# Kernel optimization log

Measured on AMD Instinct MI355X. Metric: run time of the kernel, lower is better.

## Reference

```python
import jax, jax.numpy as jnp
import numpy as np


def setup_inputs() -> dict:
    key = jax.random.key(0)
    k1, k2, k3, k4 = jax.random.split(key, 4)
    B, S, D = 16, 1024, 300      # batch, set_size, word_vector_dim
    K = 64                        # hidden_set_size == compressed_dim (element_dim)
    O = 256                       # set_representation_dim (output_dim)
    Xs = jax.random.normal(k1, (B, S, D), dtype=jnp.float32)
    # Linear(word_vector_dim -> hidden_set_size)
    W = jax.random.normal(k2, (K, D), dtype=jnp.float32) * (1.0 / np.sqrt(D))
    b = jax.random.normal(k3, (K,), dtype=jnp.float32) * 0.01
    # hidden_sets: (output_dim, hidden_set_size, element_dim) with xavier-normal scale
    xav = np.sqrt(2.0 / (K + K))
    hidden_sets = jax.random.normal(k4, (O, K, K), dtype=jnp.float32) * xav
    return {"Xs": Xs, "W": W, "b": b, "hidden_sets": hidden_sets}


def reference(Xs, W, b, hidden_sets):
    # compress: [B,S,D] @ [D,K] + b -> [B,S,K]
    Xc = jnp.einsum('bsd,kd->bsk', Xs, W) + b
    # bipartite_match: tensordot over element_dim -> [B,S,O,N] (N = hidden_set_size)
    G = jax.nn.relu(jnp.einsum('bsk,onk->bson', Xc, hidden_sets))
    # set_size (1024) > hidden_set_size (64): max over hidden-set axis, sum over set axis
    value = jnp.sum(jnp.max(G, axis=-1), axis=1)  # [B,O]
    return value
```

## Files before the change

### kernel.cpp

```cpp
#include <hip/hip_runtime.h>
#include <hip/hip_bf16.h>

#define B_  16
#define S_  1024
#define D_  300
#define DP  320
#define K_  64
#define O_  256
#define M_  (B_*S_)

typedef __attribute__((ext_vector_type(8)))  short s8b;
typedef __attribute__((ext_vector_type(4)))  float f32x4;
typedef __attribute__((ext_vector_type(16))) float f32x16;

#define MFMA16(a,b,c) __builtin_amdgcn_mfma_f32_16x16x32_bf16((a),(b),(c),0,0,0)
#define MFMA32(a,b,c) __builtin_amdgcn_mfma_f32_32x32x16_bf16((a),(b),(c),0,0,0)

__device__ __forceinline__ unsigned short bf16_bits(float f) {
    return __builtin_bit_cast(unsigned short, __float2bfloat16(f));
}

#define XS_BLK 2560
#define H_BLK  512
#define W_BLK  10
__global__ __launch_bounds__(256) void k_convert(
        const float* __restrict__ Xs, const float* __restrict__ W,
        const float* __restrict__ H,
        __hip_bfloat16* __restrict__ Xsb, __hip_bfloat16* __restrict__ Wb,
        __hip_bfloat16* __restrict__ Hb) {
    int bx = blockIdx.x, t = threadIdx.x;
    const float* src; __hip_bfloat16* dst; int r, c;
    if (bx < XS_BLK) {
        int g = bx * 256 + t;
        r = g / 40; c = (g - r * 40) * 8;
        src = Xs + (size_t)r * D_; dst = Xsb + (size_t)r * DP + c;
    } else if (bx < XS_BLK + H_BLK) {
        int g = ((bx - XS_BLK) * 256 + t) * 8;
        float4 f0 = *(const float4*)(H + g);
        float4 f1 = *(const float4*)(H + g + 4);
        union { unsigned short us[8]; uint4 q; } pk;
        pk.us[0]=bf16_bits(f0.x); pk.us[1]=bf16_bits(f0.y);
        pk.us[2]=bf16_bits(f0.z); pk.us[3]=bf16_bits(f0.w);
        pk.us[4]=bf16_bits(f1.x); pk.us[5]=bf16_bits(f1.y);
        pk.us[6]=bf16_bits(f1.z); pk.us[7]=bf16_bits(f1.w);
        *(uint4*)(Hb + g) = pk.q;
        return;
    } else {
        int g = (bx - XS_BLK - H_BLK) * 256 + t;
        r = g / 40; c = (g - r * 40) * 8;
        src = W + (size_t)r * D_; dst = Wb + (size_t)r * DP + c;
    }
    float v[8];
    if (c + 8 <= D_) {
        float4 f0 = *(const float4*)(src + c);
        float4 f1 = *(const float4*)(src + c + 4);
        v[0]=f0.x; v[1]=f0.y; v[2]=f0.z; v[3]=f0.w;
        v[4]=f1.x; v[5]=f1.y; v[6]=f1.z; v[7]=f1.w;
    } else {
#pragma unroll
        for (int j = 0; j < 8; ++j) v[j] = (c + j < D_) ? src[c + j] : 0.0f;
    }
    union { unsigned short us[8]; uint4 q; } pk;
#pragma unroll
    for (int j = 0; j < 8; ++j) pk.us[j] = bf16_bits(v[j]);
    *(uint4*)dst = pk.q;
}

__global__ __launch_bounds__(256) void k_compress(
        const __hip_bfloat16* __restrict__ Xsb,
        const __hip_bfloat16* __restrict__ Wb,
        const float* __restrict__ bias,
        __hip_bfloat16* __restrict__ Xc) {
    int tid  = threadIdx.x;
    int w    = tid >> 6, lane = tid & 63;
    int q    = lane >> 4, r = lane & 15;
    int row0 = blockIdx.x * 16;
    int col0 = w * 16;

    f32x4 acc0 = {0.f,0.f,0.f,0.f}, acc1 = {0.f,0.f,0.f,0.f};
    const __hip_bfloat16* arow = Xsb + (size_t)(row0 + r) * DP;
    const __hip_bfloat16* brow = Wb  + (size_t)(col0 + r) * DP;

#pragma unroll
    for (int ks = 0; ks < 5; ++ks) {
        int k0 = (2 * ks) * 32 + q * 8;
        int k1 = (2 * ks + 1) * 32 + q * 8;
        s8b a0 = __builtin_bit_cast(s8b, *(const uint4*)(arow + k0));
        s8b b0 = __builtin_bit_cast(s8b, *(const uint4*)(brow + k0));
        acc0 = MFMA16(a0, b0, acc0);
        s8b a1 = __builtin_bit_cast(s8b, *(const uint4*)(arow + k1));
        s8b b1 = __builtin_bit_cast(s8b, *(const uint4*)(brow + k1));
        acc1 = MFMA16(a1, b1, acc1);
    }
#pragma unroll
    for (int i = 0; i < 4; ++i) {
        int orow = row0 + q * 4 + i;
        int c    = col0 + r;
        Xc[(size_t)orow * K_ + c] =
            __float2bfloat16(acc0[i] + acc1[i] + bias[c]);
    }
}

__global__ __launch_bounds__(256, 4) void k_fused(
        const __hip_bfloat16* __restrict__ Xc,
        const __hip_bfloat16* __restrict__ Hb,
        float* __restrict__ out) {
    __shared__ __hip_bfloat16 lx[256 * 64];
    int tid   = threadIdx.x;
    int w     = tid >> 6, lane = tid & 63;
    int half  = lane >> 5, l31 = lane & 31;
    int bx    = blockIdx.x;
    int rb    = bx >> 6;
    int oq    = bx & 63;
    int o     = oq * 4 + w;
    int row0  = rb * 256;
    int batch = rb >> 2;

    {
        int r0 = tid >> 3, c = tid & 7;
#pragma unroll
        for (int i = 0; i < 8; ++i) {
            int r = r0 + i * 32;
            uint4 v = *(const uint4*)(Xc + (size_t)(row0 + r) * 64 + c * 8);
            *(uint4*)(&lx[r * 64 + (c ^ (r & 7)) * 8]) = v;
        }
    }

    s8b af[2][4];
#pragma unroll
    for (int nt = 0; nt < 2; ++nt) {
        const __hip_bfloat16* hrow =
            Hb + (size_t)(o * 64 + nt * 32 + l31) * 64 + half * 8;
#pragma unroll
        for (int ks = 0; ks < 4; ++ks)
            af[nt][ks] = __builtin_bit_cast(s8b, *(const uint4*)(hrow + ks * 16));
    }
    __syncthreads();

    float total = 0.0f;
#pragma unroll
    for (int t = 0; t < 8; ++t) {
        int rr = t * 32 + l31;
        int sw = rr & 7;
        s8b bf[4];
#pragma unroll
        for (int ks = 0; ks < 4; ++ks)
            bf[ks] = __builtin_bit_cast(s8b,
                *(const uint4*)(&lx[rr * 64 + ((2 * ks + half) ^ sw) * 8]));

        f32x16 a0 = {0.f,0.f,0.f,0.f,0.f,0.f,0.f,0.f,
                     0.f,0.f,0.f,0.f,0.f,0.f,0.f,0.f};
        f32x16 a1 = a0;
#pragma unroll
        for (int ks = 0; ks < 4; ++ks) {
            a0 = MFMA32(af[0][ks], bf[ks], a0);
            a1 = MFMA32(af[1][ks], bf[ks], a1);
        }
        float m0 = fmaxf(fmaxf(a0[0], a0[1]),  fmaxf(a0[2], a0[3]));
        float m1 = fmaxf(fmaxf(a0[4], a0[5]),  fmaxf(a0[6], a0[7]));
        float m2 = fmaxf(fmaxf(a0[8], a0[9]),  fmaxf(a0[10], a0[11]));
        float m3 = fmaxf(fmaxf(a0[12], a0[13]),fmaxf(a0[14], a0[15]));
        float n0 = fmaxf(fmaxf(a1[0], a1[1]),  fmaxf(a1[2], a1[3]));
        float n1 = fmaxf(fmaxf(a1[4], a1[5]),  fmaxf(a1[6], a1[7]));
        float n2 = fmaxf(fmaxf(a1[8], a1[9]),  fmaxf(a1[10], a1[11]));
        float n3 = fmaxf(fmaxf(a1[12], a1[13]),fmaxf(a1[14], a1[15]));
        float v  = fmaxf(fmaxf(fmaxf(m0, m1), fmaxf(m2, m3)),
                         fmaxf(fmaxf(n0, n1), fmaxf(n2, n3)));
        v = fmaxf(v, __shfl_xor(v, 32));
        v = fmaxf(v, 0.0f);
        total += v;
    }
    total += __shfl_xor(total, 1);
    total += __shfl_xor(total, 2);
    total += __shfl_xor(total, 4);
    total += __shfl_xor(total, 8);
    total += __shfl_xor(total, 16);
    if (lane == 0) atomicAdd(out + batch * O_ + o, total);
}

extern "C" void kernel_launch(void* const* d_in, const int* in_sizes, int n_in,
                              void* d_out, int out_size, void* d_ws, size_t ws_size,
                              hipStream_t stream) {
    const float* Xs   = (const float*)d_in[0];
    const float* W    = (const float*)d_in[1];
    const float* bias = (const float*)d_in[2];
    const float* H    = (const float*)d_in[3];
    float* out = (float*)d_out;

    char* ws = (char*)d_ws;
    __hip_bfloat16* Xsb = (__hip_bfloat16*)(ws);
    __hip_bfloat16* Wb  = (__hip_bfloat16*)(ws + 10485760);
    __hip_bfloat16* Hb  = (__hip_bfloat16*)(ws + 10526720);
    __hip_bfloat16* Xc  = (__hip_bfloat16*)(ws + 12623872);

    hipMemsetAsync(d_out, 0, (size_t)out_size * sizeof(float), stream);
    k_convert <<<XS_BLK + H_BLK + W_BLK, 256, 0, stream>>>(Xs, W, H, Xsb, Wb, Hb);
    k_compress<<<M_ / 16, 256, 0, stream>>>(Xsb, Wb, bias, Xc);
    k_fused   <<<64 * 64, 256, 0, stream>>>(Xc, Hb, out);
}
```

Before: 125.5 us.

## Fuse Xs bf16 conversion into compress and loop fused kernel over whole batch

```diff
diff --git a/kernel.cpp b/kernel.cpp
--- a/kernel.cpp
+++ b/kernel.cpp
@@ -20,22 +20,14 @@
     return __builtin_bit_cast(unsigned short, __float2bfloat16(f));
 }
 
-#define XS_BLK 2560
 #define H_BLK  512
 #define W_BLK  10
 __global__ __launch_bounds__(256) void k_convert(
-        const float* __restrict__ Xs, const float* __restrict__ W,
-        const float* __restrict__ H,
-        __hip_bfloat16* __restrict__ Xsb, __hip_bfloat16* __restrict__ Wb,
-        __hip_bfloat16* __restrict__ Hb) {
+        const float* __restrict__ W, const float* __restrict__ H,
+        __hip_bfloat16* __restrict__ Wb, __hip_bfloat16* __restrict__ Hb) {
     int bx = blockIdx.x, t = threadIdx.x;
-    const float* src; __hip_bfloat16* dst; int r, c;
-    if (bx < XS_BLK) {
-        int g = bx * 256 + t;
-        r = g / 40; c = (g - r * 40) * 8;
-        src = Xs + (size_t)r * D_; dst = Xsb + (size_t)r * DP + c;
-    } else if (bx < XS_BLK + H_BLK) {
-        int g = ((bx - XS_BLK) * 256 + t) * 8;
+    if (bx < H_BLK) {
+        int g = (bx * 256 + t) * 8;
         float4 f0 = *(const float4*)(H + g);
         float4 f1 = *(const float4*)(H + g + 4);
         union { unsigned short us[8]; uint4 q; } pk;
@@ -45,11 +37,10 @@
         pk.us[6]=bf16_bits(f1.z); pk.us[7]=bf16_bits(f1.w);
         *(uint4*)(Hb + g) = pk.q;
         return;
-    } else {
-        int g = (bx - XS_BLK - H_BLK) * 256 + t;
-        r = g / 40; c = (g - r * 40) * 8;
-        src = W + (size_t)r * D_; dst = Wb + (size_t)r * DP + c;
-    }
+    }
+    int g = (bx - H_BLK) * 256 + t;
+    int r = g / 40, c = (g - r * 40) * 8;
+    const float* src = W + (size_t)r * D_;
     float v[8];
     if (c + 8 <= D_) {
         float4 f0 = *(const float4*)(src + c);
@@ -63,11 +54,11 @@
     union { unsigned short us[8]; uint4 q; } pk;
 #pragma unroll
     for (int j = 0; j < 8; ++j) pk.us[j] = bf16_bits(v[j]);
-    *(uint4*)dst = pk.q;
+    *(uint4*)(Wb + (size_t)r * DP + c) = pk.q;
 }
 
 __global__ __launch_bounds__(256) void k_compress(
-        const __hip_bfloat16* __restrict__ Xsb,
+        const float* __restrict__ Xs,
         const __hip_bfloat16* __restrict__ Wb,
         const float* __restrict__ bias,
         __hip_bfloat16* __restrict__ Xc) {
@@ -78,19 +69,23 @@
     int col0 = w * 16;
 
     f32x4 acc0 = {0.f,0.f,0.f,0.f}, acc1 = {0.f,0.f,0.f,0.f};
-    const __hip_bfloat16* arow = Xsb + (size_t)(row0 + r) * DP;
-    const __hip_bfloat16* brow = Wb  + (size_t)(col0 + r) * DP;
-
-#pragma unroll
-    for (int ks = 0; ks < 5; ++ks) {
-        int k0 = (2 * ks) * 32 + q * 8;
-        int k1 = (2 * ks + 1) * 32 + q * 8;
-        s8b a0 = __builtin_bit_cast(s8b, *(const uint4*)(arow + k0));
-        s8b b0 = __builtin_bit_cast(s8b, *(const uint4*)(brow + k0));
-        acc0 = MFMA16(a0, b0, acc0);
-        s8b a1 = __builtin_bit_cast(s8b, *(const uint4*)(arow + k1));
-        s8b b1 = __builtin_bit_cast(s8b, *(const uint4*)(brow + k1));
-        acc1 = MFMA16(a1, b1, acc1);
+    const float*          arow = Xs + (size_t)(row0 + r) * D_;
+    const __hip_bfloat16* brow = Wb + (size_t)(col0 + r) * DP;
+    const float4 z4 = {0.f,0.f,0.f,0.f};
+
+#pragma unroll
+    for (int ks = 0; ks < 10; ++ks) {
+        int k0 = ks * 32 + q * 8;
+        float4 f0 = (k0     < D_) ? *(const float4*)(arow + k0)     : z4;
+        float4 f1 = (k0 + 4 < D_) ? *(const float4*)(arow + k0 + 4) : z4;
+        union { unsigned short us[8]; s8b v; } pk;
+        pk.us[0]=bf16_bits(f0.x); pk.us[1]=bf16_bits(f0.y);
+        pk.us[2]=bf16_bits(f0.z); pk.us[3]=bf16_bits(f0.w);
+        pk.us[4]=bf16_bits(f1.x); pk.us[5]=bf16_bits(f1.y);
+        pk.us[6]=bf16_bits(f1.z); pk.us[7]=bf16_bits(f1.w);
+        s8b b = __builtin_bit_cast(s8b, *(const uint4*)(brow + k0));
+        if (ks & 1) acc1 = MFMA16(pk.v, b, acc1);
+        else        acc0 = MFMA16(pk.v, b, acc0);
     }
 #pragma unroll
     for (int i = 0; i < 4; ++i) {
@@ -105,26 +100,14 @@
         const __hip_bfloat16* __restrict__ Xc,
         const __hip_bfloat16* __restrict__ Hb,
         float* __restrict__ out) {
-    __shared__ __hip_bfloat16 lx[256 * 64];
+    __shared__ __hip_bfloat16 lx[128 * 64];
     int tid   = threadIdx.x;
     int w     = tid >> 6, lane = tid & 63;
     int half  = lane >> 5, l31 = lane & 31;
     int bx    = blockIdx.x;
-    int rb    = bx >> 6;
+    int batch = bx >> 6;
     int oq    = bx & 63;
     int o     = oq * 4 + w;
-    int row0  = rb * 256;
-    int batch = rb >> 2;
-
-    {
-        int r0 = tid >> 3, c = tid & 7;
-#pragma unroll
-        for (int i = 0; i < 8; ++i) {
-            int r = r0 + i * 32;
-            uint4 v = *(const uint4*)(Xc + (size_t)(row0 + r) * 64 + c * 8);
-            *(uint4*)(&lx[r * 64 + (c ^ (r & 7)) * 8]) = v;
-        }
-    }
 
     s8b af[2][4];
 #pragma unroll
@@ -135,47 +118,74 @@
         for (int ks = 0; ks < 4; ++ks)
             af[nt][ks] = __builtin_bit_cast(s8b, *(const uint4*)(hrow + ks * 16));
     }
-    __syncthreads();
+
+    int sr = tid >> 3, sc = tid & 7;
+    const __hip_bfloat16* xbase = Xc + (size_t)batch * S_ * K_;
+
+#pragma unroll
+    for (int i = 0; i < 4; ++i) {
+        int r = sr + i * 32;
+        uint4 v = *(const uint4*)(xbase + (size_t)r * 64 + sc * 8);
+        *(uint4*)(&lx[r * 64 + (sc ^ (r & 7)) * 8]) = v;
+    }
 
     float total = 0.0f;
-#pragma unroll
-    for (int t = 0; t < 8; ++t) {
-        int rr = t * 32 + l31;
-        int sw = rr & 7;
-        s8b bf[4];
-#pragma unroll
-        for (int ks = 0; ks < 4; ++ks)
-            bf[ks] = __builtin_bit_cast(s8b,
-                *(const uint4*)(&lx[rr * 64 + ((2 * ks + half) ^ sw) * 8]));
-
-        f32x16 a0 = {0.f,0.f,0.f,0.f,0.f,0.f,0.f,0.f,
-                     0.f,0.f,0.f,0.f,0.f,0.f,0.f,0.f};
-        f32x16 a1 = a0;
-#pragma unroll
-        for (int ks = 0; ks < 4; ++ks) {
-            a0 = MFMA32(af[0][ks], bf[ks], a0);
-            a1 = MFMA32(af[1][ks], bf[ks], a1);
+    for (int it = 0; it < 8; ++it) {
+        __syncthreads();
+        uint4 npf[4];
+        if (it < 7) {
+            const __hip_bfloat16* nsrc = xbase + (size_t)(it + 1) * 128 * 64;
+#pragma unroll
+            for (int i = 0; i < 4; ++i)
+                npf[i] = *(const uint4*)(nsrc + (size_t)(sr + i * 32) * 64 + sc * 8);
         }
-        float m0 = fmaxf(fmaxf(a0[0], a0[1]),  fmaxf(a0[2], a0[3]));
-        float m1 = fmaxf(fmaxf(a0[4], a0[5]),  fmaxf(a0[6], a0[7]));
-        float m2 = fmaxf(fmaxf(a0[8], a0[9]),  fmaxf(a0[10], a0[11]));
-        float m3 = fmaxf(fmaxf(a0[12], a0[13]),fmaxf(a0[14], a0[15]));
-        float n0 = fmaxf(fmaxf(a1[0], a1[1]),  fmaxf(a1[2], a1[3]));
-        float n1 = fmaxf(fmaxf(a1[4], a1[5]),  fmaxf(a1[6], a1[7]));
-        float n2 = fmaxf(fmaxf(a1[8], a1[9]),  fmaxf(a1[10], a1[11]));
-        float n3 = fmaxf(fmaxf(a1[12], a1[13]),fmaxf(a1[14], a1[15]));
-        float v  = fmaxf(fmaxf(fmaxf(m0, m1), fmaxf(m2, m3)),
-                         fmaxf(fmaxf(n0, n1), fmaxf(n2, n3)));
-        v = fmaxf(v, __shfl_xor(v, 32));
-        v = fmaxf(v, 0.0f);
-        total += v;
+#pragma unroll
+        for (int t = 0; t < 4; ++t) {
+            int rr = t * 32 + l31;
+            int sw = rr & 7;
+            s8b bf[4];
+#pragma unroll
+            for (int ks = 0; ks < 4; ++ks)
+                bf[ks] = __builtin_bit_cast(s8b,
+                    *(const uint4*)(&lx[rr * 64 + ((2 * ks + half) ^ sw) * 8]));
+
+            f32x16 a0 = {0.f,0.f,0.f,0.f,0.f,0.f,0.f,0.f,
+                         0.f,0.f,0.f,0.f,0.f,0.f,0.f,0.f};
+            f32x16 a1 = a0;
+#pragma unroll
+            for (int ks = 0; ks < 4; ++ks) {
+                a0 = MFMA32(af[0][ks], bf[ks], a0);
+                a1 = MFMA32(af[1][ks], bf[ks], a1);
+            }
+            float m0 = fmaxf(fmaxf(a0[0], a0[1]),  fmaxf(a0[2], a0[3]));
+            float m1 = fmaxf(fmaxf(a0[4], a0[5]),  fmaxf(a0[6], a0[7]));
+            float m2 = fmaxf(fmaxf(a0[8], a0[9]),  fmaxf(a0[10], a0[11]));
+            float m3 = fmaxf(fmaxf(a0[12], a0[13]),fmaxf(a0[14], a0[15]));
+            float n0 = fmaxf(fmaxf(a1[0], a1[1]),  fmaxf(a1[2], a1[3]));
+            float n1 = fmaxf(fmaxf(a1[4], a1[5]),  fmaxf(a1[6], a1[7]));
+            float n2 = fmaxf(fmaxf(a1[8], a1[9]),  fmaxf(a1[10], a1[11]));
+            float n3 = fmaxf(fmaxf(a1[12], a1[13]),fmaxf(a1[14], a1[15]));
+            float v  = fmaxf(fmaxf(fmaxf(m0, m1), fmaxf(m2, m3)),
+                             fmaxf(fmaxf(n0, n1), fmaxf(n2, n3)));
+            v = fmaxf(v, __shfl_xor(v, 32));
+            v = fmaxf(v, 0.0f);
+            total += v;
+        }
+        __syncthreads();
+        if (it < 7) {
+#pragma unroll
+            for (int i = 0; i < 4; ++i) {
+                int r = sr + i * 32;
+                *(uint4*)(&lx[r * 64 + (sc ^ (r & 7)) * 8]) = npf[i];
+            }
+        }
     }
     total += __shfl_xor(total, 1);
     total += __shfl_xor(total, 2);
     total += __shfl_xor(total, 4);
     total += __shfl_xor(total, 8);
     total += __shfl_xor(total, 16);
-    if (lane == 0) atomicAdd(out + batch * O_ + o, total);
+    if (lane == 0) out[batch * O_ + o] = total;
 }
 
 extern "C" void kernel_launch(void* const* d_in, const int* in_sizes, int n_in,
@@ -188,13 +198,11 @@
     float* out = (float*)d_out;
 
     char* ws = (char*)d_ws;
-    __hip_bfloat16* Xsb = (__hip_bfloat16*)(ws);
-    __hip_bfloat16* Wb  = (__hip_bfloat16*)(ws + 10485760);
-    __hip_bfloat16* Hb  = (__hip_bfloat16*)(ws + 10526720);
-    __hip_bfloat16* Xc  = (__hip_bfloat16*)(ws + 12623872);
-
-    hipMemsetAsync(d_out, 0, (size_t)out_size * sizeof(float), stream);
-    k_convert <<<XS_BLK + H_BLK + W_BLK, 256, 0, stream>>>(Xs, W, H, Xsb, Wb, Hb);
-    k_compress<<<M_ / 16, 256, 0, stream>>>(Xsb, Wb, bias, Xc);
-    k_fused   <<<64 * 64, 256, 0, stream>>>(Xc, Hb, out);
-}
+    __hip_bfloat16* Wb = (__hip_bfloat16*)(ws);
+    __hip_bfloat16* Hb = (__hip_bfloat16*)(ws + 40960);
+    __hip_bfloat16* Xc = (__hip_bfloat16*)(ws + 2138112);
+
+    k_convert <<<H_BLK + W_BLK, 256, 0, stream>>>(W, H, Wb, Hb);
+    k_compress<<<M_ / 16, 256, 0, stream>>>(Xs, Wb, bias, Xc);
+    k_fused   <<<B_ * (O_ / 4), 256, 0, stream>>>(Xc, Hb, out);
+}
```

Result: no change. 123.9 us (-1.3%).
